# Optimization experiments

Measured on AMD Instinct MI355X. Metric: run time of the kernel, lower is better.

The kernel has to match this reference:

```python
import jax, jax.numpy as jnp
import numpy as np

N, F, R, H, C = 16384, 128, 16, 8, 64
E = 163840
SELF_LOOP_FILL = 0.5
NEG_SLOPE = 0.2


def _glorot(key, shape):
    fan = shape[0] + shape[-1]
    lim = jnp.sqrt(6.0 / fan)
    return jax.random.uniform(key, shape, jnp.float32, -lim, lim)


def setup_inputs() -> dict:
    key = jax.random.key(0)
    ks = jax.random.split(key, 20)
    inp = {
        'x': jax.random.normal(ks[0], (N, F), jnp.float32),
        'edge_index': jax.random.randint(ks[1], (2, E), 0, N, jnp.int64),
        'edge_attr': jax.random.uniform(ks[2], (E, R), jnp.float32),
        # layer 1 (concat=True): in=F, out per head=C, heads=H
        'Wl1': _glorot(ks[3], (F, H * C)), 'bl1': jnp.zeros((H * C,), jnp.float32),
        'Wr1': _glorot(ks[4], (F, H * C)), 'br1': jnp.zeros((H * C,), jnp.float32),
        'We1': _glorot(ks[5], (R, H * C)),
        'att1': _glorot(ks[6], (H, C)),
        'bias1': jnp.zeros((H * C,), jnp.float32),
        # layer 2 (concat=False): in=H*C
        'Wl2': _glorot(ks[7], (H * C, H * C)), 'bl2': jnp.zeros((H * C,), jnp.float32),
        'Wr2': _glorot(ks[8], (H * C, H * C)), 'br2': jnp.zeros((H * C,), jnp.float32),
        'We2': _glorot(ks[9], (R, H * C)),
        'att2': _glorot(ks[10], (H, C)),
        'bias2': jnp.zeros((C,), jnp.float32),
    }
    return inp


def gatv2_layer(x, src, dst, e, Wl, bl, Wr, br, We, att, bias, concat):
    n = x.shape[0]
    h, c = att.shape
    xl = (x @ Wl + bl).reshape(n, h, c)   # source transform (used for messages)
    xr = (x @ Wr + br).reshape(n, h, c)   # target transform
    ep = (e @ We).reshape(-1, h, c)       # edge feature transform [E',H,C]
    z = jax.nn.leaky_relu(xl[src] + xr[dst] + ep, NEG_SLOPE)  # [E',H,C]
    logits = jnp.einsum('ehc,hc->eh', z, att)                 # [E',H]
    # softmax over incoming edges of each destination node
    m = jax.ops.segment_max(logits, dst, num_segments=n)
    m = jax.lax.stop_gradient(jnp.where(jnp.isfinite(m), m, 0.0))
    ex = jnp.exp(logits - m[dst])
    denom = jax.ops.segment_sum(ex, dst, num_segments=n)
    alpha = ex / (denom[dst] + 1e-16)                         # [E',H]
    out = jax.ops.segment_sum(xl[src] * alpha[..., None], dst, num_segments=n)  # [N,H,C]
    out = out.reshape(n, h * c) if concat else out.mean(axis=1)
    return out + bias


def reference(x, edge_index, edge_attr, Wl1, bl1, Wr1, br1, We1, att1, bias1,
              Wl2, bl2, Wr2, br2, We2, att2, bias2):
    n = x.shape[0]
    loops = jnp.arange(n, dtype=edge_index.dtype)
    src = jnp.concatenate([edge_index[0], loops])
    dst = jnp.concatenate([edge_index[1], loops])
    e = jnp.concatenate([edge_attr, jnp.full((n, edge_attr.shape[1]), SELF_LOOP_FILL, edge_attr.dtype)])
    out = gatv2_layer(x, src, dst, e, Wl1, bl1, Wr1, br1, We1, att1, bias1, concat=True)
    out = gatv2_layer(out, src, dst, e, Wl2, bl2, Wr2, br2, We2, att2, bias2, concat=False)
    return out
```

## Files before the change

kernel.cpp:

```cpp
#include <hip/hip_runtime.h>
#include <cstdint>

#define NN 16384
#define FF 128
#define RR 16
#define HH 8
#define CC 64
#define HC 512
#define NC 1024
#define EE 163840
#define ET (EE + NN)

typedef __attribute__((ext_vector_type(2))) float f32x2;
typedef __attribute__((ext_vector_type(4))) float f32x4;
typedef __attribute__((ext_vector_type(8))) short short8;

__device__ __forceinline__ unsigned short f2bf(float f) {
  unsigned u = __builtin_bit_cast(unsigned, f);
  u = (u + 0x7FFFu + ((u >> 16) & 1u)) >> 16;
  return (unsigned short)u;
}
__device__ __forceinline__ float bf2f(unsigned short b) {
  unsigned u = ((unsigned)b) << 16;
  return __builtin_bit_cast(float, u);
}

__device__ __forceinline__ void gl_lds16(const void* g, void* l) {
  __builtin_amdgcn_global_load_lds(
      (const __attribute__((address_space(1))) unsigned int*)g,
      (__attribute__((address_space(3))) unsigned int*)l, 16, 0, 0);
}

__global__ __launch_bounds__(256) void count_kernel(const int* __restrict__ ei,
                                                    int* __restrict__ counts) {
  int e = blockIdx.x * 256 + threadIdx.x;
  if (e >= ET) return;
  int d = (e < EE) ? ei[EE + e] : (e - EE);
  atomicAdd(&counts[d], 1);
}

__global__ __launch_bounds__(1024) void scan_kernel(const int* __restrict__ counts,
                                                    int* __restrict__ offs,
                                                    int* __restrict__ cursor) {
  __shared__ int part[1024];
  int t = threadIdx.x;
  int base = t * 16;
  int loc[16];
  int s = 0;
#pragma unroll
  for (int i = 0; i < 16; ++i) { loc[i] = s; s += counts[base + i]; }
  part[t] = s;
  __syncthreads();
  for (int off = 1; off < 1024; off <<= 1) {
    int v = (t >= off) ? part[t - off] : 0;
    __syncthreads();
    part[t] += v;
    __syncthreads();
  }
  int excl = part[t] - s;
#pragma unroll
  for (int i = 0; i < 16; ++i) {
    int o = excl + loc[i];
    offs[base + i] = o;
    cursor[base + i] = o;
  }
  if (t == 1023) offs[NN] = part[1023];
}

__global__ __launch_bounds__(256) void scatter_kernel(const int* __restrict__ ei,
                                                      int* __restrict__ cursor,
                                                      int* __restrict__ csr,
                                                      int* __restrict__ srcc,
                                                      int* __restrict__ dstc) {
  int e = blockIdx.x * 256 + threadIdx.x;
  if (e >= ET) return;
  int s, d;
  if (e < EE) { s = ei[e]; d = ei[EE + e]; }
  else        { s = d = e - EE; }
  int p = atomicAdd(&cursor[d], 1);
  csr[p] = e;
  srcc[p] = s;
  dstc[p] = d;
}

__global__ __launch_bounds__(256) void pack_a_kernel(const float* __restrict__ A,
                                                     unsigned short* __restrict__ Ah,
                                                     unsigned short* __restrict__ Al,
                                                     int K) {
  int nkb = K >> 5;
  int rb = blockIdx.x / nkb, kb = blockIdx.x % nkb;
  int t = threadIdx.x;
  size_t obase = ((size_t)rb * nkb + kb) * 4096;
#pragma unroll
  for (int u = 0; u < 2; ++u) {
    int lin = t + u * 256;
    int r = lin >> 2, ch = lin & 3;
    int chs = (ch + (r >> 1)) & 3;
    const float* src = &A[(size_t)(rb * 128 + r) * K + kb * 32 + ch * 8];
    float4 v0 = *(const float4*)src;
    float4 v1 = *(const float4*)(src + 4);
    float v[8] = {v0.x, v0.y, v0.z, v0.w, v1.x, v1.y, v1.z, v1.w};
    short8 hv, lv;
#pragma unroll
    for (int j = 0; j < 8; ++j) {
      unsigned short h = f2bf(v[j]);
      unsigned short l = f2bf(v[j] - bf2f(h));
      hv[j] = (short)h; lv[j] = (short)l;
    }
    size_t o = obase + (size_t)r * 32 + chs * 8;
    *(short8*)&Ah[o] = hv;
    *(short8*)&Al[o] = lv;
  }
}

__global__ __launch_bounds__(256) void pack_w_kernel(const float* __restrict__ Wl,
                                                     const float* __restrict__ Wr,
                                                     unsigned short* __restrict__ Bh,
                                                     unsigned short* __restrict__ Bl,
                                                     int K) {
  int nkb = K >> 5;
  int nb = blockIdx.x / nkb, kb = blockIdx.x % nkb;
  int t = threadIdx.x;
  size_t obase = ((size_t)nb * nkb + kb) * 4096;
#pragma unroll
  for (int u = 0; u < 2; ++u) {
    int lin = t + u * 256;
    int n = lin >> 2, ch = lin & 3;
    int chs = (ch + (n >> 1)) & 3;
    int gn = nb * 128 + n;
    const float* W = (gn < HC) ? Wl : Wr;
    int cn = gn & (HC - 1);
    short8 hv, lv;
#pragma unroll
    for (int j = 0; j < 8; ++j) {
      float f = W[(size_t)(kb * 32 + ch * 8 + j) * HC + cn];
      unsigned short h = f2bf(f);
      unsigned short l = f2bf(f - bf2f(h));
      hv[j] = (short)h; lv[j] = (short)l;
    }
    size_t o = obase + (size_t)n * 32 + chs * 8;
    *(short8*)&Bh[o] = hv;
    *(short8*)&Bl[o] = lv;
  }
}

__global__ __launch_bounds__(256) void pack_wet_kernel(const float* __restrict__ We,
                                                       float* __restrict__ WeT) {
  int i = blockIdx.x * 256 + threadIdx.x;
  int c = i >> 4, r = i & 15;
  WeT[i] = We[r * HC + c];
}

__global__ __launch_bounds__(256) void gemm_mfma_kernel(const unsigned short* __restrict__ Ah,
                                                        const unsigned short* __restrict__ Al,
                                                        const unsigned short* __restrict__ Bh,
                                                        const unsigned short* __restrict__ Bl,
                                                        const float* __restrict__ bl,
                                                        const float* __restrict__ br,
                                                        float* __restrict__ C, int K) {
  __shared__ unsigned short lAh[4096], lAl[4096], lBh[4096], lBl[4096];
  int tid = threadIdx.x;
  int wave = tid >> 6, lane = tid & 63;
  int l15 = lane & 15, quad = lane >> 4;
  int wm = wave >> 1, wn = wave & 1;
  int nb = blockIdx.x, rb = blockIdx.y;
  int nkb = K >> 5;

  const unsigned short* src = (wave == 0) ? Ah : (wave == 1) ? Al : (wave == 2) ? Bh : Bl;
  unsigned short* dst = (wave == 0) ? lAh : (wave == 1) ? lAl : (wave == 2) ? lBh : lBl;
  int blk = (wave < 2) ? rb : nb;
  size_t gstep = 4096;
  const unsigned short* gbase = src + ((size_t)blk * nkb) * gstep + lane * 8;

  f32x4 acc[4][4];
#pragma unroll
  for (int i = 0; i < 4; ++i)
#pragma unroll
    for (int j = 0; j < 4; ++j) acc[i][j] = (f32x4){0.f, 0.f, 0.f, 0.f};

  int offA[4], offB[4];
#pragma unroll
  for (int t = 0; t < 4; ++t) {
    int ra = wm * 64 + t * 16 + l15;
    offA[t] = ra * 32 + ((quad + (ra >> 1)) & 3) * 8;
    int rbn = wn * 64 + t * 16 + l15;
    offB[t] = rbn * 32 + ((quad + (rbn >> 1)) & 3) * 8;
  }

  for (int kb = 0; kb < nkb; ++kb) {
    const unsigned short* g = gbase + (size_t)kb * gstep;
#pragma unroll
    for (int i = 0; i < 8; ++i)
      gl_lds16(g + i * 512, dst + i * 512);
    __syncthreads();

    short8 ah[4], al_[4], bh[4], bl_[4];
#pragma unroll
    for (int t = 0; t < 4; ++t) {
      ah[t]  = *(const short8*)&lAh[offA[t]];
      al_[t] = *(const short8*)&lAl[offA[t]];
      bh[t]  = *(const short8*)&lBh[offB[t]];
      bl_[t] = *(const short8*)&lBl[offB[t]];
    }
#pragma unroll
    for (int tm = 0; tm < 4; ++tm)
#pragma unroll
      for (int tn = 0; tn < 4; ++tn) {
        acc[tm][tn] = __builtin_amdgcn_mfma_f32_16x16x32_bf16(ah[tm], bh[tn], acc[tm][tn], 0, 0, 0);
        acc[tm][tn] = __builtin_amdgcn_mfma_f32_16x16x32_bf16(ah[tm], bl_[tn], acc[tm][tn], 0, 0, 0);
        acc[tm][tn] = __builtin_amdgcn_mfma_f32_16x16x32_bf16(al_[tm], bh[tn], acc[tm][tn], 0, 0, 0);
      }
    __syncthreads();
  }

#pragma unroll
  for (int tm = 0; tm < 4; ++tm) {
    int row = rb * 128 + wm * 64 + tm * 16 + quad * 4;
#pragma unroll
    for (int tn = 0; tn < 4; ++tn) {
      int col = nb * 128 + wn * 64 + tn * 16 + l15;
      float bias = (col < HC) ? bl[col] : br[col - HC];
#pragma unroll
      for (int r = 0; r < 4; ++r)
        C[(size_t)(row + r) * NC + col] = acc[tm][tn][r] + bias;
    }
  }
}

__global__ __launch_bounds__(256)
__attribute__((amdgpu_waves_per_eu(8, 8)))
void edge_logits_kernel(const int* __restrict__ csr,
                        const int* __restrict__ srcc,
                        const int* __restrict__ dstc,
                        const float* __restrict__ eattr,
                        const float* __restrict__ WeT,
                        const float* __restrict__ att,
                        const float* __restrict__ xlr,
                        float* __restrict__ logitsc) {
  __shared__ float se[64][16];
  __shared__ int ssrc[64];
  __shared__ int sdst[64];
  __shared__ int sedge[64];
  int t = threadIdx.x;
  int base = blockIdx.x * 64;
  int c0 = t * 2;
  f32x2 wf0[8], wf1[8];
  {
    const f32x2* w0 = (const f32x2*)&WeT[(size_t)c0 * RR];
    const f32x2* w1 = (const f32x2*)&WeT[(size_t)(c0 + 1) * RR];
#pragma unroll
    for (int j = 0; j < 8; ++j) { wf0[j] = w0[j]; wf1[j] = w1[j]; }
  }
#pragma unroll
  for (int j = 0; j < 8; ++j) {
    asm volatile("" : "+v"(wf0[j]), "+v"(wf1[j]));
  }
  float2 amv = *(const float2*)&att[c0];
  if (t < 64) {
    int i = base + t;
    sedge[t] = csr[i];
    ssrc[t] = srcc[i];
    sdst[t] = dstc[i];
  }
  __syncthreads();
  {
    int k = t >> 2, r0 = (t & 3) * 4;
    int e = sedge[k];
    float4 v;
    if (e < EE) v = *(const float4*)&eattr[(size_t)e * RR + r0];
    else        v = make_float4(0.5f, 0.5f, 0.5f, 0.5f);
    se[k][r0 + 0] = v.x; se[k][r0 + 1] = v.y;
    se[k][r0 + 2] = v.z; se[k][r0 + 3] = v.w;
  }
  __syncthreads();
  int h = t >> 5;
#pragma unroll 2
  for (int k = 0; k < 64; ++k) {
    int s = ssrc[k], d = sdst[k];
    f32x2 lv = *(const f32x2*)&xlr[(size_t)s * NC + c0];
    f32x2 rv = *(const f32x2*)&xlr[(size_t)d * NC + HC + c0];
    const f32x2* sk2 = (const f32x2*)se[k];
    f32x2 epp0 = (f32x2){0.f, 0.f};
    f32x2 epp1 = (f32x2){0.f, 0.f};
#pragma unroll
    for (int j = 0; j < 8; ++j) {
      f32x2 er2 = sk2[j];
      epp0 = __builtin_elementwise_fma(er2, wf0[j], epp0);
      epp1 = __builtin_elementwise_fma(er2, wf1[j], epp1);
    }
    f32x2 base2 = lv + rv;
    float z0 = base2.x + (epp0.x + epp0.y);
    float z1 = base2.y + (epp1.x + epp1.y);
    z0 = fmaf(0.2f, fminf(z0, 0.f), fmaxf(z0, 0.f));
    z1 = fmaf(0.2f, fminf(z1, 0.f), fmaxf(z1, 0.f));
    float p = fmaf(z0, amv.x, z1 * amv.y);
    p += __shfl_xor(p, 1);
    p += __shfl_xor(p, 2);
    p += __shfl_xor(p, 4);
    p += __shfl_xor(p, 8);
    p += __shfl_xor(p, 16);
    if ((t & 31) == 0) logitsc[(size_t)(base + k) * 8 + h] = p;
  }
}

__global__ __launch_bounds__(256) void softmax_kernel(const int* __restrict__ offs,
                                                      float* __restrict__ logitsc) {
  int lane = threadIdx.x & 63;
  int n = blockIdx.x * 4 + (threadIdx.x >> 6);
  int h = lane & 7, i0 = lane >> 3;
  int beg = offs[n], end = offs[n + 1];
  float m = -1e30f;
  for (int i = beg + i0; i < end; i += 8) m = fmaxf(m, logitsc[(size_t)i * 8 + h]);
  m = fmaxf(m, __shfl_xor(m, 8));
  m = fmaxf(m, __shfl_xor(m, 16));
  m = fmaxf(m, __shfl_xor(m, 32));
  float s = 0.f;
  for (int i = beg + i0; i < end; i += 8) {
    size_t idx = (size_t)i * 8 + h;
    float v = __expf(logitsc[idx] - m);
    logitsc[idx] = v;
    s += v;
  }
  s += __shfl_xor(s, 8);
  s += __shfl_xor(s, 16);
  s += __shfl_xor(s, 32);
  float inv = 1.f / (s + 1e-16f);
  for (int i = beg + i0; i < end; i += 8) {
    size_t idx = (size_t)i * 8 + h;
    logitsc[idx] *= inv;
  }
}

__global__ __launch_bounds__(256) void aggregate_concat_kernel(const int* __restrict__ srcc,
                                                               const int* __restrict__ offs,
                                                               const float* __restrict__ alphac,
                                                               const float* __restrict__ xlr,
                                                               const float* __restrict__ bias,
                                                               unsigned short* __restrict__ Ah2,
                                                               unsigned short* __restrict__ Al2) {
  int n = blockIdx.x, t = threadIdx.x;
  int beg = offs[n], end = offs[n + 1];
  int c0 = t, c1 = t + 256;
  int h0 = t >> 6, h1 = h0 + 4;
  float acc0 = 0.f, acc1 = 0.f;
#pragma unroll 2
  for (int i = beg; i < end; ++i) {
    int s = srcc[i];
    float a0 = alphac[(size_t)i * 8 + h0];
    float a1 = alphac[(size_t)i * 8 + h1];
    acc0 += a0 * xlr[(size_t)s * NC + c0];
    acc1 += a1 * xlr[(size_t)s * NC + c1];
  }
  float v0 = acc0 + bias[c0];
  float v1 = acc1 + bias[c1];
  int r = n & 127, rbk = n >> 7;
#pragma unroll
  for (int u = 0; u < 2; ++u) {
    int c = u ? c1 : c0;
    float v = u ? v1 : v0;
    int kb = c >> 5, ch = (c >> 3) & 3, j = c & 7;
    int chs = (ch + (r >> 1)) & 3;
    size_t idx = ((size_t)rbk * 16 + kb) * 4096 + (size_t)r * 32 + chs * 8 + j;
    unsigned short h = f2bf(v);
    Ah2[idx] = h;
    Al2[idx] = f2bf(v - bf2f(h));
  }
}

__global__ __launch_bounds__(256) void aggregate_mean_kernel(const int* __restrict__ srcc,
                                                             const int* __restrict__ offs,
                                                             const float* __restrict__ alphac,
                                                             const float* __restrict__ xlr,
                                                             const float* __restrict__ bias2,
                                                             float* __restrict__ out) {
  __shared__ float red[HC];
  int n = blockIdx.x, t = threadIdx.x;
  int beg = offs[n], end = offs[n + 1];
  int c0 = t, c1 = t + 256;
  int h0 = t >> 6, h1 = h0 + 4;
  float acc0 = 0.f, acc1 = 0.f;
#pragma unroll 2
  for (int i = beg; i < end; ++i) {
    int s = srcc[i];
    float a0 = alphac[(size_t)i * 8 + h0];
    float a1 = alphac[(size_t)i * 8 + h1];
    acc0 += a0 * xlr[(size_t)s * NC + c0];
    acc1 += a1 * xlr[(size_t)s * NC + c1];
  }
  red[c0] = acc0;
  red[c1] = acc1;
  __syncthreads();
  if (t < CC) {
    float ssum = 0.f;
#pragma unroll
    for (int hh = 0; hh < HH; ++hh) ssum += red[hh * CC + t];
    out[(size_t)n * CC + t] = ssum * 0.125f + bias2[t];
  }
}

extern "C" void kernel_launch(void* const* d_in, const int* in_sizes, int n_in,
                              void* d_out, int out_size, void* d_ws, size_t ws_size,
                              hipStream_t stream) {
  const float* x     = (const float*)d_in[0];
  const int*   ei    = (const int*)d_in[1];
  const float* eattr = (const float*)d_in[2];
  const float* Wl1   = (const float*)d_in[3];
  const float* bl1   = (const float*)d_in[4];
  const float* Wr1   = (const float*)d_in[5];
  const float* br1   = (const float*)d_in[6];
  const float* We1   = (const float*)d_in[7];
  const float* att1  = (const float*)d_in[8];
  const float* bias1 = (const float*)d_in[9];
  const float* Wl2   = (const float*)d_in[10];
  const float* bl2   = (const float*)d_in[11];
  const float* Wr2   = (const float*)d_in[12];
  const float* br2   = (const float*)d_in[13];
  const float* We2   = (const float*)d_in[14];
  const float* att2  = (const float*)d_in[15];
  const float* bias2 = (const float*)d_in[16];
  float* out = (float*)d_out;

  char* ws = (char*)d_ws;
  size_t off = 0;
  auto alloc = [&](size_t bytes) {
    char* p = ws + off;
    off += (bytes + 255) & ~(size_t)255;
    return p;
  };
  float* bufC = (float*)alloc((size_t)NN * NC * 4);
  float* logits = (float*)alloc((size_t)ET * HH * 4);
  unsigned short* Ah1 = (unsigned short*)alloc((size_t)NN * FF * 2);
  unsigned short* Al1 = (unsigned short*)alloc((size_t)NN * FF * 2);
  unsigned short* Ah2 = (unsigned short*)alloc((size_t)NN * HC * 2);
  unsigned short* Al2 = (unsigned short*)alloc((size_t)NN * HC * 2);
  unsigned short* Wh1 = (unsigned short*)alloc((size_t)FF * NC * 2);
  unsigned short* Wlo1 = (unsigned short*)alloc((size_t)FF * NC * 2);
  unsigned short* Wh2 = (unsigned short*)alloc((size_t)HC * NC * 2);
  unsigned short* Wlo2 = (unsigned short*)alloc((size_t)HC * NC * 2);
  float* WeT1 = (float*)alloc((size_t)HC * RR * 4);
  float* WeT2 = (float*)alloc((size_t)HC * RR * 4);
  int* counts = (int*)alloc((size_t)NN * 4);
  int* offs   = (int*)alloc((size_t)(NN + 1) * 4);
  int* cursor = (int*)alloc((size_t)NN * 4);
  int* csr    = (int*)alloc((size_t)ET * 4);
  int* srcc   = (int*)alloc((size_t)ET * 4);
  int* dstc   = (int*)alloc((size_t)ET * 4);
  (void)ws_size; (void)in_sizes; (void)n_in; (void)out_size;

  hipMemsetAsync(counts, 0, (size_t)NN * 4, stream);
  int eb = (ET + 255) / 256;
  count_kernel<<<eb, 256, 0, stream>>>(ei, counts);
  scan_kernel<<<1, 1024, 0, stream>>>(counts, offs, cursor);
  scatter_kernel<<<eb, 256, 0, stream>>>(ei, cursor, csr, srcc, dstc);

  pack_a_kernel<<<(NN / 128) * (FF / 32), 256, 0, stream>>>(x, Ah1, Al1, FF);
  pack_w_kernel<<<(NC / 128) * (FF / 32), 256, 0, stream>>>(Wl1, Wr1, Wh1, Wlo1, FF);
  pack_w_kernel<<<(NC / 128) * (HC / 32), 256, 0, stream>>>(Wl2, Wr2, Wh2, Wlo2, HC);
  pack_wet_kernel<<<(HC * RR) / 256, 256, 0, stream>>>(We1, WeT1);
  pack_wet_kernel<<<(HC * RR) / 256, 256, 0, stream>>>(We2, WeT2);

  dim3 ggrid(NC / 128, NN / 128);
  int elb = ET / 64;

  gemm_mfma_kernel<<<ggrid, 256, 0, stream>>>(Ah1, Al1, Wh1, Wlo1, bl1, br1, bufC, FF);
  edge_logits_kernel<<<elb, 256, 0, stream>>>(csr, srcc, dstc, eattr, WeT1, att1, bufC, logits);
  softmax_kernel<<<NN / 4, 256, 0, stream>>>(offs, logits);
  aggregate_concat_kernel<<<NN, 256, 0, stream>>>(srcc, offs, logits, bufC, bias1, Ah2, Al2);

  gemm_mfma_kernel<<<ggrid, 256, 0, stream>>>(Ah2, Al2, Wh2, Wlo2, bl2, br2, bufC, HC);
  edge_logits_kernel<<<elb, 256, 0, stream>>>(csr, srcc, dstc, eattr, WeT2, att2, bufC, logits);
  softmax_kernel<<<NN / 4, 256, 0, stream>>>(offs, logits);
  aggregate_mean_kernel<<<NN, 256, 0, stream>>>(srcc, offs, logits, bufC, bias2, out);
}
```

Measured before the change: 515.3 us.

## Fuse edge logits, softmax and aggregation into one online-softmax per-node kernel

Replaces the three-kernel sequence (edge logits, segment softmax, aggregation) with a single kernel per destination node that computes logits and runs an online softmax with running max and rescaled accumulator. This removes the logits buffer round-trips, two launches per layer and the dstc array, and loads the target row once per node. In exchange, each block loops serially over a node's in-edges and reloads the edge-attribute row per edge from global memory in every thread, and adds two exps per edge per thread. The degree-driven per-block work may be imbalanced.

```diff
diff --git a/kernel.cpp b/kernel.cpp
--- a/kernel.cpp
+++ b/kernel.cpp
@@ -70,8 +70,7 @@
 __global__ __launch_bounds__(256) void scatter_kernel(const int* __restrict__ ei,
                                                       int* __restrict__ cursor,
                                                       int* __restrict__ csr,
-                                                      int* __restrict__ srcc,
-                                                      int* __restrict__ dstc) {
+                                                      int* __restrict__ srcc) {
   int e = blockIdx.x * 256 + threadIdx.x;
   if (e >= ET) return;
   int s, d;
@@ -80,7 +79,6 @@
   int p = atomicAdd(&cursor[d], 1);
   csr[p] = e;
   srcc[p] = s;
-  dstc[p] = d;
 }
 
 __global__ __launch_bounds__(256) void pack_a_kernel(const float* __restrict__ A,
@@ -227,23 +225,15 @@
   }
 }
 
-__global__ __launch_bounds__(256)
-__attribute__((amdgpu_waves_per_eu(8, 8)))
-void edge_logits_kernel(const int* __restrict__ csr,
-                        const int* __restrict__ srcc,
-                        const int* __restrict__ dstc,
-                        const float* __restrict__ eattr,
-                        const float* __restrict__ WeT,
-                        const float* __restrict__ att,
-                        const float* __restrict__ xlr,
-                        float* __restrict__ logitsc) {
-  __shared__ float se[64][16];
-  __shared__ int ssrc[64];
-  __shared__ int sdst[64];
-  __shared__ int sedge[64];
-  int t = threadIdx.x;
-  int base = blockIdx.x * 64;
+
+__device__ __forceinline__ void fused_edge_body(
+    const int* __restrict__ csr, const int* __restrict__ srcc,
+    const int* __restrict__ offs, const float* __restrict__ eattr,
+    const float* __restrict__ WeT, const float* __restrict__ att,
+    const float* __restrict__ xlr, int n, int t,
+    float& out0, float& out1) {
   int c0 = t * 2;
+  int beg = offs[n], end = offs[n + 1];
   f32x2 wf0[8], wf1[8];
   {
     const f32x2* w0 = (const f32x2*)&WeT[(size_t)c0 * RR];
@@ -251,42 +241,30 @@
 #pragma unroll
     for (int j = 0; j < 8; ++j) { wf0[j] = w0[j]; wf1[j] = w1[j]; }
   }
-#pragma unroll
-  for (int j = 0; j < 8; ++j) {
-    asm volatile("" : "+v"(wf0[j]), "+v"(wf1[j]));
-  }
   float2 amv = *(const float2*)&att[c0];
-  if (t < 64) {
-    int i = base + t;
-    sedge[t] = csr[i];
-    ssrc[t] = srcc[i];
-    sdst[t] = dstc[i];
-  }
-  __syncthreads();
-  {
-    int k = t >> 2, r0 = (t & 3) * 4;
-    int e = sedge[k];
-    float4 v;
-    if (e < EE) v = *(const float4*)&eattr[(size_t)e * RR + r0];
-    else        v = make_float4(0.5f, 0.5f, 0.5f, 0.5f);
-    se[k][r0 + 0] = v.x; se[k][r0 + 1] = v.y;
-    se[k][r0 + 2] = v.z; se[k][r0 + 3] = v.w;
-  }
-  __syncthreads();
-  int h = t >> 5;
+  f32x2 rv = *(const f32x2*)&xlr[(size_t)n * NC + HC + c0];
+  float m = -1e30f, l = 0.f;
+  f32x2 acc = (f32x2){0.f, 0.f};
 #pragma unroll 2
-  for (int k = 0; k < 64; ++k) {
-    int s = ssrc[k], d = sdst[k];
+  for (int i = beg; i < end; ++i) {
+    int e = csr[i];
+    int s = srcc[i];
     f32x2 lv = *(const f32x2*)&xlr[(size_t)s * NC + c0];
-    f32x2 rv = *(const f32x2*)&xlr[(size_t)d * NC + HC + c0];
-    const f32x2* sk2 = (const f32x2*)se[k];
+    f32x2 e2[8];
+    if (e < EE) {
+      const f32x2* ep2 = (const f32x2*)&eattr[(size_t)e * RR];
+#pragma unroll
+      for (int j = 0; j < 8; ++j) e2[j] = ep2[j];
+    } else {
+#pragma unroll
+      for (int j = 0; j < 8; ++j) e2[j] = (f32x2){0.5f, 0.5f};
+    }
     f32x2 epp0 = (f32x2){0.f, 0.f};
     f32x2 epp1 = (f32x2){0.f, 0.f};
 #pragma unroll
     for (int j = 0; j < 8; ++j) {
-      f32x2 er2 = sk2[j];
-      epp0 = __builtin_elementwise_fma(er2, wf0[j], epp0);
-      epp1 = __builtin_elementwise_fma(er2, wf1[j], epp1);
+      epp0 = __builtin_elementwise_fma(e2[j], wf0[j], epp0);
+      epp1 = __builtin_elementwise_fma(e2[j], wf1[j], epp1);
     }
     f32x2 base2 = lv + rv;
     float z0 = base2.x + (epp0.x + epp0.y);
@@ -299,64 +277,35 @@
     p += __shfl_xor(p, 4);
     p += __shfl_xor(p, 8);
     p += __shfl_xor(p, 16);
-    if ((t & 31) == 0) logitsc[(size_t)(base + k) * 8 + h] = p;
-  }
-}
-
-__global__ __launch_bounds__(256) void softmax_kernel(const int* __restrict__ offs,
-                                                      float* __restrict__ logitsc) {
-  int lane = threadIdx.x & 63;
-  int n = blockIdx.x * 4 + (threadIdx.x >> 6);
-  int h = lane & 7, i0 = lane >> 3;
-  int beg = offs[n], end = offs[n + 1];
-  float m = -1e30f;
-  for (int i = beg + i0; i < end; i += 8) m = fmaxf(m, logitsc[(size_t)i * 8 + h]);
-  m = fmaxf(m, __shfl_xor(m, 8));
-  m = fmaxf(m, __shfl_xor(m, 16));
-  m = fmaxf(m, __shfl_xor(m, 32));
-  float s = 0.f;
-  for (int i = beg + i0; i < end; i += 8) {
-    size_t idx = (size_t)i * 8 + h;
-    float v = __expf(logitsc[idx] - m);
-    logitsc[idx] = v;
-    s += v;
-  }
-  s += __shfl_xor(s, 8);
-  s += __shfl_xor(s, 16);
-  s += __shfl_xor(s, 32);
-  float inv = 1.f / (s + 1e-16f);
-  for (int i = beg + i0; i < end; i += 8) {
-    size_t idx = (size_t)i * 8 + h;
-    logitsc[idx] *= inv;
-  }
-}
-
-__global__ __launch_bounds__(256) void aggregate_concat_kernel(const int* __restrict__ srcc,
-                                                               const int* __restrict__ offs,
-                                                               const float* __restrict__ alphac,
-                                                               const float* __restrict__ xlr,
-                                                               const float* __restrict__ bias,
-                                                               unsigned short* __restrict__ Ah2,
-                                                               unsigned short* __restrict__ Al2) {
+    float nm = fmaxf(m, p);
+    float sc = __expf(m - nm);
+    float el = __expf(p - nm);
+    l = l * sc + el;
+    acc.x = acc.x * sc + el * lv.x;
+    acc.y = acc.y * sc + el * lv.y;
+    m = nm;
+  }
+  float inv = 1.f / (l + 1e-16f);
+  out0 = acc.x * inv;
+  out1 = acc.y * inv;
+}
+
+__global__ __launch_bounds__(256) void fused_concat_kernel(
+    const int* __restrict__ csr, const int* __restrict__ srcc,
+    const int* __restrict__ offs, const float* __restrict__ eattr,
+    const float* __restrict__ WeT, const float* __restrict__ att,
+    const float* __restrict__ xlr, const float* __restrict__ bias,
+    unsigned short* __restrict__ Ah2, unsigned short* __restrict__ Al2) {
   int n = blockIdx.x, t = threadIdx.x;
-  int beg = offs[n], end = offs[n + 1];
-  int c0 = t, c1 = t + 256;
-  int h0 = t >> 6, h1 = h0 + 4;
-  float acc0 = 0.f, acc1 = 0.f;
-#pragma unroll 2
-  for (int i = beg; i < end; ++i) {
-    int s = srcc[i];
-    float a0 = alphac[(size_t)i * 8 + h0];
-    float a1 = alphac[(size_t)i * 8 + h1];
-    acc0 += a0 * xlr[(size_t)s * NC + c0];
-    acc1 += a1 * xlr[(size_t)s * NC + c1];
-  }
-  float v0 = acc0 + bias[c0];
-  float v1 = acc1 + bias[c1];
+  float o0, o1;
+  fused_edge_body(csr, srcc, offs, eattr, WeT, att, xlr, n, t, o0, o1);
+  int c0 = t * 2;
+  float v0 = o0 + bias[c0];
+  float v1 = o1 + bias[c0 + 1];
   int r = n & 127, rbk = n >> 7;
 #pragma unroll
   for (int u = 0; u < 2; ++u) {
-    int c = u ? c1 : c0;
+    int c = c0 + u;
     float v = u ? v1 : v0;
     int kb = c >> 5, ch = (c >> 3) & 3, j = c & 7;
     int chs = (ch + (r >> 1)) & 3;
@@ -367,28 +316,19 @@
   }
 }
 
-__global__ __launch_bounds__(256) void aggregate_mean_kernel(const int* __restrict__ srcc,
-                                                             const int* __restrict__ offs,
-                                                             const float* __restrict__ alphac,
-                                                             const float* __restrict__ xlr,
-                                                             const float* __restrict__ bias2,
-                                                             float* __restrict__ out) {
+__global__ __launch_bounds__(256) void fused_mean_kernel(
+    const int* __restrict__ csr, const int* __restrict__ srcc,
+    const int* __restrict__ offs, const float* __restrict__ eattr,
+    const float* __restrict__ WeT, const float* __restrict__ att,
+    const float* __restrict__ xlr, const float* __restrict__ bias2,
+    float* __restrict__ out) {
   __shared__ float red[HC];
   int n = blockIdx.x, t = threadIdx.x;
-  int beg = offs[n], end = offs[n + 1];
-  int c0 = t, c1 = t + 256;
-  int h0 = t >> 6, h1 = h0 + 4;
-  float acc0 = 0.f, acc1 = 0.f;
-#pragma unroll 2
-  for (int i = beg; i < end; ++i) {
-    int s = srcc[i];
-    float a0 = alphac[(size_t)i * 8 + h0];
-    float a1 = alphac[(size_t)i * 8 + h1];
-    acc0 += a0 * xlr[(size_t)s * NC + c0];
-    acc1 += a1 * xlr[(size_t)s * NC + c1];
-  }
-  red[c0] = acc0;
-  red[c1] = acc1;
+  float o0, o1;
+  fused_edge_body(csr, srcc, offs, eattr, WeT, att, xlr, n, t, o0, o1);
+  int c0 = t * 2;
+  red[c0] = o0;
+  red[c0 + 1] = o1;
   __syncthreads();
   if (t < CC) {
     float ssum = 0.f;
@@ -428,7 +368,6 @@
     return p;
   };
   float* bufC = (float*)alloc((size_t)NN * NC * 4);
-  float* logits = (float*)alloc((size_t)ET * HH * 4);
   unsigned short* Ah1 = (unsigned short*)alloc((size_t)NN * FF * 2);
   unsigned short* Al1 = (unsigned short*)alloc((size_t)NN * FF * 2);
   unsigned short* Ah2 = (unsigned short*)alloc((size_t)NN * HC * 2);
@@ -444,14 +383,13 @@
   int* cursor = (int*)alloc((size_t)NN * 4);
   int* csr    = (int*)alloc((size_t)ET * 4);
   int* srcc   = (int*)alloc((size_t)ET * 4);
-  int* dstc   = (int*)alloc((size_t)ET * 4);
   (void)ws_size; (void)in_sizes; (void)n_in; (void)out_size;
 
   hipMemsetAsync(counts, 0, (size_t)NN * 4, stream);
   int eb = (ET + 255) / 256;
   count_kernel<<<eb, 256, 0, stream>>>(ei, counts);
   scan_kernel<<<1, 1024, 0, stream>>>(counts, offs, cursor);
-  scatter_kernel<<<eb, 256, 0, stream>>>(ei, cursor, csr, srcc, dstc);
+  scatter_kernel<<<eb, 256, 0, stream>>>(ei, cursor, csr, srcc);
 
   pack_a_kernel<<<(NN / 128) * (FF / 32), 256, 0, stream>>>(x, Ah1, Al1, FF);
   pack_w_kernel<<<(NC / 128) * (FF / 32), 256, 0, stream>>>(Wl1, Wr1, Wh1, Wlo1, FF);
@@ -460,15 +398,10 @@
   pack_wet_kernel<<<(HC * RR) / 256, 256, 0, stream>>>(We2, WeT2);
 
   dim3 ggrid(NC / 128, NN / 128);
-  int elb = ET / 64;
 
   gemm_mfma_kernel<<<ggrid, 256, 0, stream>>>(Ah1, Al1, Wh1, Wlo1, bl1, br1, bufC, FF);
-  edge_logits_kernel<<<elb, 256, 0, stream>>>(csr, srcc, dstc, eattr, WeT1, att1, bufC, logits);
-  softmax_kernel<<<NN / 4, 256, 0, stream>>>(offs, logits);
-  aggregate_concat_kernel<<<NN, 256, 0, stream>>>(srcc, offs, logits, bufC, bias1, Ah2, Al2);
+  fused_concat_kernel<<<NN, 256, 0, stream>>>(csr, srcc, offs, eattr, WeT1, att1, bufC, bias1, Ah2, Al2);
 
   gemm_mfma_kernel<<<ggrid, 256, 0, stream>>>(Ah2, Al2, Wh2, Wlo2, bl2, br2, bufC, HC);
-  edge_logits_kernel<<<elb, 256, 0, stream>>>(csr, srcc, dstc, eattr, WeT2, att2, bufC, logits);
-  softmax_kernel<<<NN / 4, 256, 0, stream>>>(offs, logits);
-  aggregate_mean_kernel<<<NN, 256, 0, stream>>>(srcc, offs, logits, bufC, bias2, out);
-}
+  fused_mean_kernel<<<NN, 256, 0, stream>>>(csr, srcc, offs, eattr, WeT2, att2, bufC, bias2, out);
+}
```

Result: faster. 462.4 us (-10.3%).
